# Kernel optimization log

Hardware: AMD Instinct MI355X
Metric: run time of the kernel (lower is better)

## Reference

```python
import jax, jax.numpy as jnp
import numpy as np

N = 50000
NEG_SLOPE = 0.2


def gat_conv(x, src, dst, W, a_src, a_dst, bias, heads, out_ch, concat):
    n = x.shape[0]
    h = (x @ W).reshape(n, heads, out_ch)            # [N, H, C]
    alpha_s = jnp.einsum('nhc,hc->nh', h, a_src)      # [N, H]
    alpha_d = jnp.einsum('nhc,hc->nh', h, a_dst)
    e = alpha_s[src] + alpha_d[dst]                   # [E, H]
    e = jax.nn.leaky_relu(e, NEG_SLOPE)
    # segment softmax over destination node (PyG: softmax over index=dst)
    m = jax.ops.segment_max(e, dst, num_segments=n)
    e = jnp.exp(e - m[dst])
    s = jax.ops.segment_sum(e, dst, num_segments=n)
    alpha = e / (s[dst] + 1e-16)                      # [E, H]
    msg = h[src] * alpha[:, :, None]                  # [E, H, C]
    out = jax.ops.segment_sum(msg, dst, num_segments=n)  # [N, H, C]
    out = out.reshape(n, heads * out_ch) if concat else out.mean(axis=1)
    return out + bias


def setup_inputs() -> dict:
    key = jax.random.key(0)
    ks = jax.random.split(key, 12)
    F_in, H, C1, NC = 512, 8, 16, 64
    E = 800000
    x = jax.random.normal(ks[0], (N, F_in), dtype=jnp.float32)
    edge_index = jax.random.randint(ks[1], (2, E), 0, N, dtype=jnp.int64)
    def glorot(k, shape):
        fan = shape[0] + shape[-1]
        lim = jnp.sqrt(6.0 / fan).astype(jnp.float32)
        return jax.random.uniform(k, shape, jnp.float32, -lim, lim)
    W1 = glorot(ks[2], (F_in, H * C1))
    att_src1 = glorot(ks[3], (H, C1))
    att_dst1 = glorot(ks[4], (H, C1))
    b1 = jnp.zeros((H * C1,), jnp.float32)
    W2 = glorot(ks[5], (H * C1, NC))
    att_src2 = glorot(ks[6], (1, NC))
    att_dst2 = glorot(ks[7], (1, NC))
    b2 = jnp.zeros((NC,), jnp.float32)
    return {"x": x, "edge_index": edge_index,
            "W1": W1, "att_src1": att_src1, "att_dst1": att_dst1, "b1": b1,
            "W2": W2, "att_src2": att_src2, "att_dst2": att_dst2, "b2": b2}


def reference(x, edge_index, W1, att_src1, att_dst1, b1, W2, att_src2, att_dst2, b2):
    # PyG GATConv default add_self_loops=True
    loops = jnp.arange(N, dtype=edge_index.dtype)
    src = jnp.concatenate([edge_index[0], loops])
    dst = jnp.concatenate([edge_index[1], loops])
    h = gat_conv(x, src, dst, W1, att_src1, att_dst1, b1, heads=8, out_ch=16, concat=True)
    h = jax.nn.relu(h)
    out = gat_conv(h, src, dst, W2, att_src2, att_dst2, b2, heads=1, out_ch=64, concat=False)
    return jax.nn.log_softmax(out, axis=1)
```

## Files before the change

kernel.cpp:

```cpp
#include <hip/hip_runtime.h>
#include <math.h>

#define N_NODES 50000
#define FIN 512
#define H1 8
#define D1 128
#define D2 64
#define NSCB ((N_NODES + 1023) >> 10)
#define GG 1563

typedef __attribute__((ext_vector_type(4))) float f32x4;
typedef __attribute__((ext_vector_type(8))) __bf16 bf16x8;
typedef __attribute__((ext_vector_type(4))) __bf16 bf16x4;

__device__ __forceinline__ void gload_lds16(const void* g, void* l) {
    __builtin_amdgcn_global_load_lds(
        (const __attribute__((address_space(1))) void*)g,
        (__attribute__((address_space(3))) void*)l, 16, 0, 0);
}

__global__ __launch_bounds__(256) void k_prep(const float* __restrict__ W1,
                                              const float* __restrict__ W2,
                                              __bf16* __restrict__ WpP,
                                              __bf16* __restrict__ Wp2,
                                              int* __restrict__ cnt) {
    int idx = blockIdx.x * 256 + threadIdx.x;
    int k = idx >> 7, col = idx & 127;
    int region = k >> 6;
    int kgl = (k >> 3) & 7;
    int u_out = (kgl * 128 + col) ^ (kgl & 3);
    WpP[region * 8192 + u_out * 8 + (k & 7)] = (__bf16)W1[idx];
    if (idx < N_NODES) cnt[idx] = 0;
    if (idx < D1 * D2) {
        int k2 = idx >> 6, col2 = idx & 63;
        Wp2[(k2 >> 3) * 512 + col2 * 8 + (k2 & 7)] = (__bf16)W2[idx];
    }
}

__global__ __launch_bounds__(256) void k_mega(const float* __restrict__ x,
                                              const __bf16* __restrict__ WpP,
                                              const float* __restrict__ asrc1,
                                              const float* __restrict__ adst1,
                                              __bf16* __restrict__ h1b,
                                              float* __restrict__ as1,
                                              float* __restrict__ ad1,
                                              const int* __restrict__ ei, int E,
                                              int* __restrict__ cnt,
                                              int* __restrict__ rank) {
    __shared__ __align__(16) __bf16 As[32 * 64];
    __shared__ __align__(16) __bf16 Bs[64 * 128];
    const int t = threadIdx.x;

    if (blockIdx.x >= GG) {
        int e = (blockIdx.x - GG) * 256 + t;
        int ET = E + N_NODES;
        if (e < ET) {
            int d = (e < E) ? ei[E + e] : (e - E);
            rank[e] = atomicAdd(&cnt[d], 1);
        }
        return;
    }

    const int l = t & 63;
    const int w = t >> 6;
    const int wr = (w >> 1) * 16, wc = (w & 1) * 64;
    const int n0 = blockIdx.x * 32;

    f32x4 acc[4];
    #pragma unroll
    for (int j = 0; j < 4; ++j) acc[j] = (f32x4){0.f, 0.f, 0.f, 0.f};

    const int arow = t >> 4;
    const int ak4  = (t & 15) * 4;

    for (int s = 0; s < 8; ++s) {
        const int k0 = s * 64;
        {
            const __bf16* gsrc = WpP + (size_t)s * 8192;
            #pragma unroll
            for (int i = 0; i < 4; ++i) {
                int ubase = w * 256 + i * 64;
                gload_lds16(gsrc + (ubase + l) * 8, Bs + ubase * 8);
            }
        }
        #pragma unroll
        for (int i = 0; i < 2; ++i) {
            int row = arow + i * 16;
            int grow = n0 + row;
            float4 f = {0.f, 0.f, 0.f, 0.f};
            if (grow < N_NODES)
                f = *(const float4*)(x + (size_t)grow * FIN + k0 + ak4);
            bf16x4 v = {(__bf16)f.x, (__bf16)f.y, (__bf16)f.z, (__bf16)f.w};
            int eo = (row * 64 + ak4) ^ ((row & 7) << 3);
            *(bf16x4*)(As + eo) = v;
        }
        __syncthreads();
        #pragma unroll
        for (int ks = 0; ks < 2; ++ks) {
            bf16x8 af, bfr[4];
            {
                int row = wr + (l & 15);
                int eo = (row * 64 + ks * 32 + (l >> 4) * 8) ^ ((row & 7) << 3);
                af = *(const bf16x8*)(As + eo);
            }
            #pragma unroll
            for (int fn = 0; fn < 4; ++fn) {
                int col = wc + fn * 16 + (l & 15);
                int kg = ks * 4 + (l >> 4);
                int u = (kg * 128 + col) ^ (kg & 3);
                bfr[fn] = *(const bf16x8*)(Bs + u * 8);
            }
            #pragma unroll
            for (int fn = 0; fn < 4; ++fn)
                acc[fn] = __builtin_amdgcn_mfma_f32_16x16x32_bf16(
                    af, bfr[fn], acc[fn], 0, 0, 0);
        }
        __syncthreads();
    }
    #pragma unroll
    for (int reg = 0; reg < 4; ++reg) {
        int row = n0 + wr + (l >> 4) * 4 + reg;
        if (row >= N_NODES) continue;
        #pragma unroll
        for (int fn = 0; fn < 4; ++fn) {
            int col = wc + fn * 16 + (l & 15);
            h1b[(size_t)row * D1 + col] = (__bf16)acc[fn][reg];
        }
    }
    const int c16 = l & 15;
    float av[4], dv[4];
    #pragma unroll
    for (int fn = 0; fn < 4; ++fn) {
        int head = (wc >> 4) + fn;
        av[fn] = asrc1[head * 16 + c16];
        dv[fn] = adst1[head * 16 + c16];
    }
    #pragma unroll
    for (int reg = 0; reg < 4; ++reg) {
        #pragma unroll
        for (int fn = 0; fn < 4; ++fn) {
            float vs = acc[fn][reg] * av[fn];
            float vd = acc[fn][reg] * dv[fn];
            #pragma unroll
            for (int mk = 1; mk <= 8; mk <<= 1) {
                vs += __shfl_xor(vs, mk, 64);
                vd += __shfl_xor(vd, mk, 64);
            }
            if (c16 == 0) {
                int row = n0 + wr + (l >> 4) * 4 + reg;
                if (row < N_NODES) {
                    int head = (wc >> 4) + fn;
                    as1[(size_t)row * 8 + head] = vs;
                    ad1[(size_t)row * 8 + head] = vd;
                }
            }
        }
    }
}

__global__ __launch_bounds__(256) void k_scan1(const int* __restrict__ cnt,
                                               int* __restrict__ basep,
                                               int* __restrict__ aux) {
    __shared__ int lds[256];
    int t = threadIdx.x, b = blockIdx.x;
    int g = b * 1024 + t * 4;
    int v0 = (g + 0 < N_NODES) ? cnt[g + 0] : 0;
    int v1 = (g + 1 < N_NODES) ? cnt[g + 1] : 0;
    int v2 = (g + 2 < N_NODES) ? cnt[g + 2] : 0;
    int v3 = (g + 3 < N_NODES) ? cnt[g + 3] : 0;
    int tsum = v0 + v1 + v2 + v3;
    lds[t] = tsum; __syncthreads();
    for (int off = 1; off < 256; off <<= 1) {
        int add = (t >= off) ? lds[t - off] : 0;
        __syncthreads();
        lds[t] += add;
        __syncthreads();
    }
    int excl = lds[t] - tsum;
    if (g + 0 < N_NODES) basep[g + 0] = excl;
    if (g + 1 < N_NODES) basep[g + 1] = excl + v0;
    if (g + 2 < N_NODES) basep[g + 2] = excl + v0 + v1;
    if (g + 3 < N_NODES) basep[g + 3] = excl + v0 + v1 + v2;
    if (t == 255) aux[b] = lds[255];
}

__global__ __launch_bounds__(64) void k_scan2(const int* __restrict__ aux,
                                              int* __restrict__ auxs) {
    int t = threadIdx.x;
    int v = (t < NSCB) ? aux[t] : 0;
    int orig = v;
    for (int off = 1; off < 64; off <<= 1) {
        int x = __shfl_up(v, off, 64);
        if (t >= off) v += x;
    }
    auxs[t] = v - orig;
}

__global__ __launch_bounds__(256) void k_scan3(int* __restrict__ basep,
                                               const int* __restrict__ auxs, int ET) {
    int i = blockIdx.x * 256 + threadIdx.x;
    if (i < N_NODES) basep[i] += auxs[i >> 10];
    if (i == 0) basep[N_NODES] = ET;
}

__global__ __launch_bounds__(256) void k_scatter(const int* __restrict__ ei, int E,
                                                 const int* __restrict__ basep,
                                                 const int* __restrict__ rank,
                                                 int* __restrict__ srcs) {
    int e = blockIdx.x * 256 + threadIdx.x;
    int ET = E + N_NODES;
    if (e >= ET) return;
    int s = (e < E) ? ei[e] : (e - E);
    int d = (e < E) ? ei[E + e] : (e - E);
    srcs[basep[d] + rank[e]] = s;
}

__global__ __launch_bounds__(256) void k_agg1(const int* __restrict__ basep,
                                              const int* __restrict__ srcs,
                                              const float* __restrict__ as1,
                                              const float* __restrict__ ad1,
                                              const __bf16* __restrict__ h1b,
                                              const float* __restrict__ b1,
                                              __bf16* __restrict__ r1b) {
    __shared__ float elds[4][512];
    const int w = threadIdx.x >> 6;
    const int l = threadIdx.x & 63;
    const int half = l >> 5;
    const int c4 = (l & 31) * 4;
    const int h = c4 >> 4;
    const int n = blockIdx.x * 4 + w;
    const int p0 = basep[n], p1 = basep[n + 1];
    const int m = p1 - p0;
    float adv[8];
    #pragma unroll
    for (int i = 0; i < 8; ++i) adv[i] = ad1[(size_t)n * 8 + i];
    float a0 = 0.f, a1 = 0.f, a2 = 0.f, a3 = 0.f, se = 0.f;
    for (int base = 0; base < m; base += 64) {
        const int cm = min(64, m - base);
        asm volatile("s_waitcnt lgkmcnt(0)" ::: "memory");
        int my_s = 0;
        if (l < cm) {
            my_s = srcs[p0 + base + l];
            const float4* ap = (const float4*)(as1 + (size_t)my_s * 8);
            float4 A0 = ap[0], A1 = ap[1];
            float uu[8] = {A0.x + adv[0], A0.y + adv[1], A0.z + adv[2], A0.w + adv[3],
                           A1.x + adv[4], A1.y + adv[5], A1.z + adv[6], A1.w + adv[7]};
            float ee[8];
            #pragma unroll
            for (int i = 0; i < 8; ++i) {
                float u = uu[i];
                u = (u > 0.f) ? u : 0.2f * u;
                ee[i] = __expf(u);
            }
            *(float4*)(&elds[w][l * 8])     = make_float4(ee[0], ee[1], ee[2], ee[3]);
            *(float4*)(&elds[w][l * 8 + 4]) = make_float4(ee[4], ee[5], ee[6], ee[7]);
        }
        asm volatile("s_waitcnt lgkmcnt(0)" ::: "memory");
        #pragma unroll 2
        for (int j2 = 0; j2 < cm; j2 += 2) {
            int j = j2 + half;
            bool ok = j < cm;
            int jj = ok ? j : 0;
            int s = __shfl(my_s, jj, 64);
            float ee = elds[w][jj * 8 + h];
            if (!ok) ee = 0.f;
            se += ee;
            bf16x4 hv = *(const bf16x4*)(h1b + (size_t)s * D1 + c4);
            a0 += ee * (float)hv.x;
            a1 += ee * (float)hv.y;
            a2 += ee * (float)hv.z;
            a3 += ee * (float)hv.w;
        }
    }
    a0 += __shfl_xor(a0, 32, 64);
    a1 += __shfl_xor(a1, 32, 64);
    a2 += __shfl_xor(a2, 32, 64);
    a3 += __shfl_xor(a3, 32, 64);
    se += __shfl_xor(se, 32, 64);
    if (half == 0) {
        float inv = 1.f / (se + 1e-16f);
        bf16x4 r = {(__bf16)fmaxf(a0 * inv + b1[c4], 0.f),
                    (__bf16)fmaxf(a1 * inv + b1[c4 + 1], 0.f),
                    (__bf16)fmaxf(a2 * inv + b1[c4 + 2], 0.f),
                    (__bf16)fmaxf(a3 * inv + b1[c4 + 3], 0.f)};
        *(bf16x4*)(r1b + (size_t)n * D1 + c4) = r;
    }
}

__global__ __launch_bounds__(256) void k_gemm2(const __bf16* __restrict__ r1b,
                                               const __bf16* __restrict__ Wp2,
                                               const float* __restrict__ av2,
                                               const float* __restrict__ dv2,
                                               __bf16* __restrict__ h2b,
                                               float* __restrict__ as2,
                                               float* __restrict__ ad2) {
    __shared__ __align__(16) __bf16 As[128 * 128];
    __shared__ __align__(16) __bf16 Bs[128 * 64];
    const int t = threadIdx.x;
    const int l = t & 63;
    const int w = t >> 6;
    const int wr = w * 32;
    const int n0 = blockIdx.x * 128;

    const uint4* gb = (const uint4*)Wp2;
    #pragma unroll
    for (int i = 0; i < 4; ++i) {
        int u = t + i * 256;
        uint4 d = gb[u];
        int u2 = u ^ ((u >> 6) & 3);
        *(uint4*)(Bs + u2 * 8) = d;
    }
    #pragma unroll
    for (int i = 0; i < 8; ++i) {
        int u = t + i * 256;
        int row = u >> 4, koff = (u & 15) * 8;
        bf16x8 v = {};
        if (n0 + row < N_NODES)
            v = *(const bf16x8*)(r1b + (size_t)(n0 + row) * D1 + koff);
        int eo = (row * 128 + koff) ^ ((row & 7) << 3);
        *(bf16x8*)(As + eo) = v;
    }
    __syncthreads();

    f32x4 acc[2][4];
    #pragma unroll
    for (int i = 0; i < 2; ++i)
        #pragma unroll
        for (int j = 0; j < 4; ++j) acc[i][j] = (f32x4){0.f, 0.f, 0.f, 0.f};

    #pragma unroll
    for (int ks = 0; ks < 4; ++ks) {
        bf16x8 af[2], bfr[4];
        #pragma unroll
        for (int fm = 0; fm < 2; ++fm) {
            int row = wr + fm * 16 + (l & 15);
            int eo = (row * 128 + ks * 32 + (l >> 4) * 8) ^ ((row & 7) << 3);
            af[fm] = *(const bf16x8*)(As + eo);
        }
        #pragma unroll
        for (int fn = 0; fn < 4; ++fn) {
            int col = fn * 16 + (l & 15);
            int kg = ks * 4 + (l >> 4);
            int u = (kg * 64 + col) ^ (kg & 3);
            bfr[fn] = *(const bf16x8*)(Bs + u * 8);
        }
        #pragma unroll
        for (int fm = 0; fm < 2; ++fm)
            #pragma unroll
            for (int fn = 0; fn < 4; ++fn)
                acc[fm][fn] = __builtin_amdgcn_mfma_f32_16x16x32_bf16(
                    af[fm], bfr[fn], acc[fm][fn], 0, 0, 0);
    }
    #pragma unroll
    for (int fm = 0; fm < 2; ++fm) {
        #pragma unroll
        for (int reg = 0; reg < 4; ++reg) {
            int row = n0 + wr + fm * 16 + (l >> 4) * 4 + reg;
            if (row >= N_NODES) continue;
            #pragma unroll
            for (int fn = 0; fn < 4; ++fn) {
                int col = fn * 16 + (l & 15);
                h2b[(size_t)row * D2 + col] = (__bf16)acc[fm][fn][reg];
            }
        }
    }
    const int c16 = l & 15;
    float av[4], dv[4];
    #pragma unroll
    for (int fn = 0; fn < 4; ++fn) {
        av[fn] = av2[fn * 16 + c16];
        dv[fn] = dv2[fn * 16 + c16];
    }
    #pragma unroll
    for (int fm = 0; fm < 2; ++fm) {
        #pragma unroll
        for (int reg = 0; reg < 4; ++reg) {
            float vs = 0.f, vd = 0.f;
            #pragma unroll
            for (int fn = 0; fn < 4; ++fn) {
                vs += acc[fm][fn][reg] * av[fn];
                vd += acc[fm][fn][reg] * dv[fn];
            }
            #pragma unroll
            for (int mk = 1; mk <= 8; mk <<= 1) {
                vs += __shfl_xor(vs, mk, 64);
                vd += __shfl_xor(vd, mk, 64);
            }
            if (c16 == 0) {
                int row = n0 + wr + fm * 16 + (l >> 4) * 4 + reg;
                if (row < N_NODES) { as2[row] = vs; ad2[row] = vd; }
            }
        }
    }
}

__global__ __launch_bounds__(256) void k_agg2(const int* __restrict__ basep,
                                              const int* __restrict__ srcs,
                                              const float* __restrict__ as2,
                                              const float* __restrict__ ad2,
                                              const __bf16* __restrict__ h2b,
                                              const float* __restrict__ b2,
                                              float* __restrict__ out) {
    const int w = threadIdx.x >> 6;
    const int l = threadIdx.x & 63;
    const int q = l >> 4;
    const int c4 = (l & 15) * 4;
    const int n = blockIdx.x * 4 + w;
    const int p0 = basep[n], p1 = basep[n + 1];
    const int m = p1 - p0;
    const float adn = ad2[n];
    float a0 = 0.f, a1 = 0.f, a2 = 0.f, a3 = 0.f, se = 0.f;
    for (int base = 0; base < m; base += 64) {
        const int cm = min(64, m - base);
        int my_s = 0; float my_e = 0.f;
        if (l < cm) {
            my_s = srcs[p0 + base + l];
            float u = as2[my_s] + adn;
            u = (u > 0.f) ? u : 0.2f * u;
            my_e = __expf(u);
        }
        #pragma unroll 2
        for (int j4 = 0; j4 < cm; j4 += 4) {
            int j = j4 + q;
            bool ok = j < cm;
            int jj = ok ? j : 0;
            int s = __shfl(my_s, jj, 64);
            float ee = __shfl(my_e, jj, 64);
            if (!ok) ee = 0.f;
            se += ee;
            bf16x4 hv = *(const bf16x4*)(h2b + (size_t)s * D2 + c4);
            a0 += ee * (float)hv.x;
            a1 += ee * (float)hv.y;
            a2 += ee * (float)hv.z;
            a3 += ee * (float)hv.w;
        }
    }
    #pragma unroll
    for (int mk = 16; mk <= 32; mk <<= 1) {
        a0 += __shfl_xor(a0, mk, 64);
        a1 += __shfl_xor(a1, mk, 64);
        a2 += __shfl_xor(a2, mk, 64);
        a3 += __shfl_xor(a3, mk, 64);
        se += __shfl_xor(se, mk, 64);
    }
    float inv = 1.f / (se + 1e-16f);
    float v0 = a0 * inv + b2[c4];
    float v1 = a1 * inv + b2[c4 + 1];
    float v2 = a2 * inv + b2[c4 + 2];
    float v3 = a3 * inv + b2[c4 + 3];
    float mx = fmaxf(fmaxf(v0, v1), fmaxf(v2, v3));
    #pragma unroll
    for (int mk = 1; mk <= 8; mk <<= 1) mx = fmaxf(mx, __shfl_xor(mx, mk, 64));
    float ex = __expf(v0 - mx) + __expf(v1 - mx) + __expf(v2 - mx) + __expf(v3 - mx);
    #pragma unroll
    for (int mk = 1; mk <= 8; mk <<= 1) ex += __shfl_xor(ex, mk, 64);
    float lse = mx + __logf(ex);
    if (q == 0) {
        float4 r = {v0 - lse, v1 - lse, v2 - lse, v3 - lse};
        *(float4*)(out + (size_t)n * D2 + c4) = r;
    }
}

extern "C" void kernel_launch(void* const* d_in, const int* in_sizes, int n_in,
                              void* d_out, int out_size, void* d_ws, size_t ws_size,
                              hipStream_t stream) {
    const float* x     = (const float*)d_in[0];
    const int*   ei    = (const int*)d_in[1];
    const float* W1    = (const float*)d_in[2];
    const float* asrc1 = (const float*)d_in[3];
    const float* adst1 = (const float*)d_in[4];
    const float* b1    = (const float*)d_in[5];
    const float* W2    = (const float*)d_in[6];
    const float* asrc2 = (const float*)d_in[7];
    const float* adst2 = (const float*)d_in[8];
    const float* b2    = (const float*)d_in[9];

    const int E  = in_sizes[1] / 2;
    const int ET = E + N_NODES;

    __bf16* r1b = (__bf16*)d_ws;
    float* fw  = (float*)(r1b + (size_t)N_NODES * D1);
    float* as1  = fw;
    float* ad1  = as1  + (size_t)N_NODES * H1;
    float* as2  = ad1  + (size_t)N_NODES * H1;
    float* ad2  = as2  + N_NODES;
    int* iw   = (int*)(ad2 + N_NODES);
    int* cnt  = iw;
    int* basep= cnt  + N_NODES;
    int* aux  = basep + N_NODES + 1;
    int* auxs = aux  + 64;
    int* rank = auxs + 64;
    int* srcs = rank + ET;
    uintptr_t pa = ((uintptr_t)(srcs + ET) + 255) & ~(uintptr_t)255;
    __bf16* WpP  = (__bf16*)pa;
    __bf16* Wp2  = WpP + (size_t)FIN * D1;
    __bf16* h1b  = Wp2 + (size_t)D1 * D2;
    __bf16* h2b  = h1b + (size_t)N_NODES * D1;

    const int gE = (ET + 255) / 256;
    const int gN = (N_NODES + 255) / 256;

    k_prep   <<<FIN * D1 / 256, 256, 0, stream>>>(W1, W2, WpP, Wp2, cnt);
    k_mega   <<<GG + gE, 256, 0, stream>>>(x, WpP, asrc1, adst1, h1b, as1, ad1,
                                           ei, E, cnt, rank);
    k_scan1  <<<NSCB, 256, 0, stream>>>(cnt, basep, aux);
    k_scan2  <<<1, 64, 0, stream>>>(aux, auxs);
    k_scan3  <<<gN, 256, 0, stream>>>(basep, auxs, ET);
    k_scatter<<<gE, 256, 0, stream>>>(ei, E, basep, rank, srcs);

    k_agg1   <<<N_NODES / 4, 256, 0, stream>>>(basep, srcs, as1, ad1, h1b, b1, r1b);
    k_gemm2  <<<(N_NODES + 127) / 128, 256, 0, stream>>>(r1b, Wp2, asrc2, adst2, h2b, as2, ad2);
    k_agg2   <<<N_NODES / 4, 256, 0, stream>>>(basep, srcs, as2, ad2, h2b, b2, (float*)d_out);
}
```

Before: 159.1 us.

## Double-buffer GEMM LDS tiles and widen aggregation gathers to 16-byte loads

The layer-1 GEMM in k_mega now uses two LDS buffers for A and B, prefetching the next k-slice from global memory while MFMAs run on the current one, which removes one barrier per step and hides load latency. Both aggregation kernels now gather 8 bf16 values per lane (16-byte loads), processing more edges per wavefront iteration, with an extra shuffle-reduction stage. The trade-off is doubled LDS use in k_mega, which may lower occupancy, plus more registers for the 8-wide accumulators.

```diff
diff --git a/kernel.cpp b/kernel.cpp
--- a/kernel.cpp
+++ b/kernel.cpp
@@ -47,8 +47,8 @@
                                               const int* __restrict__ ei, int E,
                                               int* __restrict__ cnt,
                                               int* __restrict__ rank) {
-    __shared__ __align__(16) __bf16 As[32 * 64];
-    __shared__ __align__(16) __bf16 Bs[64 * 128];
+    __shared__ __align__(16) __bf16 As[2][32 * 64];
+    __shared__ __align__(16) __bf16 Bs[2][64 * 128];
     const int t = threadIdx.x;
 
     if (blockIdx.x >= GG) {
@@ -73,47 +73,80 @@
     const int arow = t >> 4;
     const int ak4  = (t & 15) * 4;
 
+    float4 fx[2];
+    {
+        const __bf16* gsrc = WpP;
+        #pragma unroll
+        for (int i = 0; i < 4; ++i) {
+            int ubase = w * 256 + i * 64;
+            gload_lds16(gsrc + (ubase + l) * 8, &Bs[0][ubase * 8]);
+        }
+        #pragma unroll
+        for (int i = 0; i < 2; ++i) {
+            int grow = n0 + arow + i * 16;
+            fx[i] = (grow < N_NODES)
+                ? *(const float4*)(x + (size_t)grow * FIN + ak4)
+                : make_float4(0.f, 0.f, 0.f, 0.f);
+        }
+        #pragma unroll
+        for (int i = 0; i < 2; ++i) {
+            int row = arow + i * 16;
+            bf16x4 v = {(__bf16)fx[i].x, (__bf16)fx[i].y,
+                        (__bf16)fx[i].z, (__bf16)fx[i].w};
+            int eo = (row * 64 + ak4) ^ ((row & 7) << 3);
+            *(bf16x4*)(&As[0][0] + eo) = v;
+        }
+    }
+    __syncthreads();
+
     for (int s = 0; s < 8; ++s) {
-        const int k0 = s * 64;
-        {
-            const __bf16* gsrc = WpP + (size_t)s * 8192;
+        const int cur = s & 1;
+        float4 nfx[2];
+        if (s < 7) {
+            const int k0 = (s + 1) * 64;
+            const __bf16* gsrc = WpP + (size_t)(s + 1) * 8192;
             #pragma unroll
             for (int i = 0; i < 4; ++i) {
                 int ubase = w * 256 + i * 64;
-                gload_lds16(gsrc + (ubase + l) * 8, Bs + ubase * 8);
-            }
-        }
-        #pragma unroll
-        for (int i = 0; i < 2; ++i) {
-            int row = arow + i * 16;
-            int grow = n0 + row;
-            float4 f = {0.f, 0.f, 0.f, 0.f};
-            if (grow < N_NODES)
-                f = *(const float4*)(x + (size_t)grow * FIN + k0 + ak4);
-            bf16x4 v = {(__bf16)f.x, (__bf16)f.y, (__bf16)f.z, (__bf16)f.w};
-            int eo = (row * 64 + ak4) ^ ((row & 7) << 3);
-            *(bf16x4*)(As + eo) = v;
-        }
-        __syncthreads();
+                gload_lds16(gsrc + (ubase + l) * 8, &Bs[cur ^ 1][ubase * 8]);
+            }
+            #pragma unroll
+            for (int i = 0; i < 2; ++i) {
+                int grow = n0 + arow + i * 16;
+                nfx[i] = (grow < N_NODES)
+                    ? *(const float4*)(x + (size_t)grow * FIN + k0 + ak4)
+                    : make_float4(0.f, 0.f, 0.f, 0.f);
+            }
+        }
         #pragma unroll
         for (int ks = 0; ks < 2; ++ks) {
             bf16x8 af, bfr[4];
             {
                 int row = wr + (l & 15);
                 int eo = (row * 64 + ks * 32 + (l >> 4) * 8) ^ ((row & 7) << 3);
-                af = *(const bf16x8*)(As + eo);
+                af = *(const bf16x8*)(&As[cur][0] + eo);
             }
             #pragma unroll
             for (int fn = 0; fn < 4; ++fn) {
                 int col = wc + fn * 16 + (l & 15);
                 int kg = ks * 4 + (l >> 4);
                 int u = (kg * 128 + col) ^ (kg & 3);
-                bfr[fn] = *(const bf16x8*)(Bs + u * 8);
+                bfr[fn] = *(const bf16x8*)(&Bs[cur][0] + u * 8);
             }
             #pragma unroll
             for (int fn = 0; fn < 4; ++fn)
                 acc[fn] = __builtin_amdgcn_mfma_f32_16x16x32_bf16(
                     af, bfr[fn], acc[fn], 0, 0, 0);
+        }
+        if (s < 7) {
+            #pragma unroll
+            for (int i = 0; i < 2; ++i) {
+                int row = arow + i * 16;
+                bf16x4 v = {(__bf16)nfx[i].x, (__bf16)nfx[i].y,
+                            (__bf16)nfx[i].z, (__bf16)nfx[i].w};
+                int eo = (row * 64 + ak4) ^ ((row & 7) << 3);
+                *(bf16x4*)(&As[cur ^ 1][0] + eo) = v;
+            }
         }
         __syncthreads();
     }
@@ -225,16 +258,17 @@
     __shared__ float elds[4][512];
     const int w = threadIdx.x >> 6;
     const int l = threadIdx.x & 63;
-    const int half = l >> 5;
-    const int c4 = (l & 31) * 4;
-    const int h = c4 >> 4;
+    const int q = l >> 4;
+    const int c8 = (l & 15) * 8;
+    const int h = (l & 15) >> 1;
     const int n = blockIdx.x * 4 + w;
     const int p0 = basep[n], p1 = basep[n + 1];
     const int m = p1 - p0;
     float adv[8];
     #pragma unroll
     for (int i = 0; i < 8; ++i) adv[i] = ad1[(size_t)n * 8 + i];
-    float a0 = 0.f, a1 = 0.f, a2 = 0.f, a3 = 0.f, se = 0.f;
+    float ac[8] = {0.f, 0.f, 0.f, 0.f, 0.f, 0.f, 0.f, 0.f};
+    float se = 0.f;
     for (int base = 0; base < m; base += 64) {
         const int cm = min(64, m - base);
         asm volatile("s_waitcnt lgkmcnt(0)" ::: "memory");
@@ -257,33 +291,32 @@
         }
         asm volatile("s_waitcnt lgkmcnt(0)" ::: "memory");
         #pragma unroll 2
-        for (int j2 = 0; j2 < cm; j2 += 2) {
-            int j = j2 + half;
+        for (int j4 = 0; j4 < cm; j4 += 4) {
+            int j = j4 + q;
             bool ok = j < cm;
             int jj = ok ? j : 0;
             int s = __shfl(my_s, jj, 64);
             float ee = elds[w][jj * 8 + h];
             if (!ok) ee = 0.f;
             se += ee;
-            bf16x4 hv = *(const bf16x4*)(h1b + (size_t)s * D1 + c4);
-            a0 += ee * (float)hv.x;
-            a1 += ee * (float)hv.y;
-            a2 += ee * (float)hv.z;
-            a3 += ee * (float)hv.w;
-        }
-    }
-    a0 += __shfl_xor(a0, 32, 64);
-    a1 += __shfl_xor(a1, 32, 64);
-    a2 += __shfl_xor(a2, 32, 64);
-    a3 += __shfl_xor(a3, 32, 64);
-    se += __shfl_xor(se, 32, 64);
-    if (half == 0) {
+            bf16x8 hv = *(const bf16x8*)(h1b + (size_t)s * D1 + c8);
+            #pragma unroll
+            for (int i = 0; i < 8; ++i) ac[i] += ee * (float)hv[i];
+        }
+    }
+    #pragma unroll
+    for (int mk = 16; mk <= 32; mk <<= 1) {
+        #pragma unroll
+        for (int i = 0; i < 8; ++i) ac[i] += __shfl_xor(ac[i], mk, 64);
+        se += __shfl_xor(se, mk, 64);
+    }
+    if (q == 0) {
         float inv = 1.f / (se + 1e-16f);
-        bf16x4 r = {(__bf16)fmaxf(a0 * inv + b1[c4], 0.f),
-                    (__bf16)fmaxf(a1 * inv + b1[c4 + 1], 0.f),
-                    (__bf16)fmaxf(a2 * inv + b1[c4 + 2], 0.f),
-                    (__bf16)fmaxf(a3 * inv + b1[c4 + 3], 0.f)};
-        *(bf16x4*)(r1b + (size_t)n * D1 + c4) = r;
+        bf16x8 r;
+        #pragma unroll
+        for (int i = 0; i < 8; ++i)
+            r[i] = (__bf16)fmaxf(ac[i] * inv + b1[c8 + i], 0.f);
+        *(bf16x8*)(r1b + (size_t)n * D1 + c8) = r;
     }
 }
 
@@ -403,13 +436,14 @@
                                               float* __restrict__ out) {
     const int w = threadIdx.x >> 6;
     const int l = threadIdx.x & 63;
-    const int q = l >> 4;
-    const int c4 = (l & 15) * 4;
+    const int o = l >> 3;
+    const int c8 = (l & 7) * 8;
     const int n = blockIdx.x * 4 + w;
     const int p0 = basep[n], p1 = basep[n + 1];
     const int m = p1 - p0;
     const float adn = ad2[n];
-    float a0 = 0.f, a1 = 0.f, a2 = 0.f, a3 = 0.f, se = 0.f;
+    float ac[8] = {0.f, 0.f, 0.f, 0.f, 0.f, 0.f, 0.f, 0.f};
+    float se = 0.f;
     for (int base = 0; base < m; base += 64) {
         const int cm = min(64, m - base);
         int my_s = 0; float my_e = 0.f;
@@ -420,44 +454,45 @@
             my_e = __expf(u);
         }
         #pragma unroll 2
-        for (int j4 = 0; j4 < cm; j4 += 4) {
-            int j = j4 + q;
+        for (int j8 = 0; j8 < cm; j8 += 8) {
+            int j = j8 + o;
             bool ok = j < cm;
             int jj = ok ? j : 0;
             int s = __shfl(my_s, jj, 64);
             float ee = __shfl(my_e, jj, 64);
             if (!ok) ee = 0.f;
             se += ee;
-            bf16x4 hv = *(const bf16x4*)(h2b + (size_t)s * D2 + c4);
-            a0 += ee * (float)hv.x;
-            a1 += ee * (float)hv.y;
-            a2 += ee * (float)hv.z;
-            a3 += ee * (float)hv.w;
-        }
-    }
-    #pragma unroll
-    for (int mk = 16; mk <= 32; mk <<= 1) {
-        a0 += __shfl_xor(a0, mk, 64);
-        a1 += __shfl_xor(a1, mk, 64);
-        a2 += __shfl_xor(a2, mk, 64);
-        a3 += __shfl_xor(a3, mk, 64);
+            bf16x8 hv = *(const bf16x8*)(h2b + (size_t)s * D2 + c8);
+            #pragma unroll
+            for (int i = 0; i < 8; ++i) ac[i] += ee * (float)hv[i];
+        }
+    }
+    #pragma unroll
+    for (int mk = 8; mk <= 32; mk <<= 1) {
+        #pragma unroll
+        for (int i = 0; i < 8; ++i) ac[i] += __shfl_xor(ac[i], mk, 64);
         se += __shfl_xor(se, mk, 64);
     }
     float inv = 1.f / (se + 1e-16f);
-    float v0 = a0 * inv + b2[c4];
-    float v1 = a1 * inv + b2[c4 + 1];
-    float v2 = a2 * inv + b2[c4 + 2];
-    float v3 = a3 * inv + b2[c4 + 3];
-    float mx = fmaxf(fmaxf(v0, v1), fmaxf(v2, v3));
-    #pragma unroll
-    for (int mk = 1; mk <= 8; mk <<= 1) mx = fmaxf(mx, __shfl_xor(mx, mk, 64));
-    float ex = __expf(v0 - mx) + __expf(v1 - mx) + __expf(v2 - mx) + __expf(v3 - mx);
-    #pragma unroll
-    for (int mk = 1; mk <= 8; mk <<= 1) ex += __shfl_xor(ex, mk, 64);
+    float v[8];
+    #pragma unroll
+    for (int i = 0; i < 8; ++i) v[i] = ac[i] * inv + b2[c8 + i];
+    float mx = v[0];
+    #pragma unroll
+    for (int i = 1; i < 8; ++i) mx = fmaxf(mx, v[i]);
+    #pragma unroll
+    for (int mk = 1; mk <= 4; mk <<= 1) mx = fmaxf(mx, __shfl_xor(mx, mk, 64));
+    float ex = 0.f;
+    #pragma unroll
+    for (int i = 0; i < 8; ++i) ex += __expf(v[i] - mx);
+    #pragma unroll
+    for (int mk = 1; mk <= 4; mk <<= 1) ex += __shfl_xor(ex, mk, 64);
     float lse = mx + __logf(ex);
-    if (q == 0) {
-        float4 r = {v0 - lse, v1 - lse, v2 - lse, v3 - lse};
-        *(float4*)(out + (size_t)n * D2 + c4) = r;
+    if (o == 0) {
+        f32x4 r0 = {v[0] - lse, v[1] - lse, v[2] - lse, v[3] - lse};
+        f32x4 r1 = {v[4] - lse, v[5] - lse, v[6] - lse, v[7] - lse};
+        *(f32x4*)(out + (size_t)n * D2 + c8)     = r0;
+        *(f32x4*)(out + (size_t)n * D2 + c8 + 4) = r1;
     }
 }
 
```

Measured after the change: 159.8 us. Within noise of the previous version (+0.4%).
